# Optimization experiments

Measured on AMD Instinct MI355X. Metric: run time of the kernel, lower is better.

The kernel has to match this reference:

```python
import jax, jax.numpy as jnp
import numpy as np

HEADS = 4
DIM_HEAD = 32


def setup_inputs() -> dict:
    key = jax.random.key(0)
    k1, k2, k3, k4 = jax.random.split(key, 4)
    dim = 64
    hidden = HEADS * DIM_HEAD  # 128
    x = jax.random.normal(k1, (1, dim, 16, 16, 16), jnp.float32)
    # Conv3d 1x1 kernels collapse to [out_ch, in_ch] matrices
    w_qkv = jax.random.normal(k2, (hidden * 3, dim), jnp.float32) * 0.05
    w_out = jax.random.normal(k3, (dim, hidden), jnp.float32) * 0.05
    b_out = jax.random.normal(k4, (dim,), jnp.float32) * 0.05
    return {"x": x, "w_qkv": w_qkv, "w_out": w_out, "b_out": b_out}


def reference(x, w_qkv, w_out, b_out):
    scale = DIM_HEAD ** -0.5
    b, c, dz, dy, dx = x.shape
    n = dz * dy * dx
    xf = x.reshape(b, c, n)  # flatten spatial dims
    # 1x1 Conv3d (no bias) == channel matmul: [b, 3*hidden, n]
    qkv = jnp.einsum('oc,bcn->bon', w_qkv, xf)
    q, k, v = jnp.split(qkv, 3, axis=1)  # each [b, hidden, n]
    def split_heads(t):
        return t.reshape(b, HEADS, DIM_HEAD, n)  # [b, h, d, n]
    q, k, v = split_heads(q), split_heads(k), split_heads(v)
    q = q * scale
    # sim[b,h,i,j] = sum_d q[b,h,d,i] k[b,h,d,j]
    sim = jnp.einsum('bhdi,bhdj->bhij', q, k)
    sim = sim - jax.lax.stop_gradient(jnp.max(sim, axis=-1, keepdims=True))
    attn = jax.nn.softmax(sim, axis=-1)
    # out[b,h,i,d] = sum_j attn[b,h,i,j] v[b,h,d,j]
    out = jnp.einsum('bhij,bhdj->bhid', attn, v)
    # 'b h (z y x) d -> b (h d) z y x'
    out = out.transpose(0, 1, 3, 2).reshape(b, HEADS * DIM_HEAD, n)
    # final 1x1 Conv3d with bias
    y = jnp.einsum('oc,bcn->bon', w_out, out) + b_out[None, :, None]
    return y.reshape(b, -1, dz, dy, dx)
```

## Files before the change

### kernel.cpp

```cpp
#include <hip/hip_runtime.h>


typedef _Float16 f16x8 __attribute__((ext_vector_type(8)));
typedef _Float16 f16x4 __attribute__((ext_vector_type(4)));
typedef _Float16 f16x2v __attribute__((ext_vector_type(2)));
typedef float f32x4 __attribute__((ext_vector_type(4)));

static __device__ inline f16x4 pack4(float a, float b, float c, float d) {
  f16x4 r;
  r.x = (_Float16)a; r.y = (_Float16)b; r.z = (_Float16)c; r.w = (_Float16)d;
  return r;
}
static __device__ inline f16x2v pack2(float a, float b) {
  f16x2v r;
  r.x = (_Float16)a; r.y = (_Float16)b;
  return r;
}

__global__ __launch_bounds__(256) void qkv_kernel(
    const float* __restrict__ x, const float* __restrict__ w,
    _Float16* __restrict__ qo, _Float16* __restrict__ ko, _Float16* __restrict__ vo)
{
  __shared__ __align__(16) float xs[64 * 68];
  __shared__ __align__(16) float wsb[32 * 68];
  const int t = threadIdx.x;
  const int n0 = blockIdx.x * 64;
  const int o0 = blockIdx.y * 32;
  #pragma unroll
  for (int i = 0; i < 4; ++i) {
    int ch = t + i * 256;
    int c = ch >> 4, p = ch & 15;
    *reinterpret_cast<float4*>(&xs[c * 68 + p * 4]) =
        *reinterpret_cast<const float4*>(&x[c * 4096 + n0 + p * 4]);
  }
  #pragma unroll
  for (int i = 0; i < 2; ++i) {
    int ch = t + i * 256;
    int o = ch >> 4, p = ch & 15;
    *reinterpret_cast<float4*>(&wsb[o * 68 + p * 4]) =
        *reinterpret_cast<const float4*>(&w[(o0 + o) * 64 + p * 4]);
  }
  __syncthreads();
  const int oL = (t >> 5) * 4;
  const int nL = (t & 31) * 2;
  float acc[4][2] = {};
  for (int c4 = 0; c4 < 64; c4 += 4) {
    float2 xa[4];
    #pragma unroll
    for (int k = 0; k < 4; ++k)
      xa[k] = *reinterpret_cast<const float2*>(&xs[(c4 + k) * 68 + nL]);
    #pragma unroll
    for (int i = 0; i < 4; ++i) {
      float4 wv = *reinterpret_cast<const float4*>(&wsb[(oL + i) * 68 + c4]);
      acc[i][0] += wv.x * xa[0].x + wv.y * xa[1].x + wv.z * xa[2].x + wv.w * xa[3].x;
      acc[i][1] += wv.x * xa[0].y + wv.y * xa[1].y + wv.z * xa[2].y + wv.w * xa[3].y;
    }
  }
  const float qs = 0.17677669529663689f * 1.4426950408889634f;
  if (o0 < 128) {
    int ho = o0 >> 5;
    #pragma unroll
    for (int j = 0; j < 2; ++j) {
      int n = n0 + nL + j;
      *reinterpret_cast<f16x4*>(&qo[(ho * 4096 + n) * 32 + oL]) =
          pack4(acc[0][j] * qs, acc[1][j] * qs, acc[2][j] * qs, acc[3][j] * qs);
    }
  } else if (o0 < 256) {
    int ho = (o0 - 128) >> 5;
    #pragma unroll
    for (int j = 0; j < 2; ++j) {
      int n = n0 + nL + j;
      *reinterpret_cast<f16x4*>(&ko[(ho * 4096 + n) * 32 + oL]) =
          pack4(acc[0][j], acc[1][j], acc[2][j], acc[3][j]);
    }
  } else {
    #pragma unroll
    for (int i = 0; i < 4; ++i) {
      *reinterpret_cast<f16x2v*>(&vo[(size_t)(o0 - 256 + oL + i) * 4096 + n0 + nL]) =
          pack2(acc[i][0], acc[i][1]);
    }
  }
}

__global__ __launch_bounds__(512, 4) void attn_kernel(
    const _Float16* __restrict__ qg, const _Float16* __restrict__ kg,
    const _Float16* __restrict__ vg, float* __restrict__ Opart,
    float* __restrict__ lpart, int jlen)
{
  __shared__ __align__(16) _Float16 Ks[2][64 * 40];
  __shared__ __align__(16) _Float16 Vs[2][32 * 72];
  const int t = threadIdx.x;
  const int ck = blockIdx.x;
  const int qt = blockIdx.y;
  const int h  = blockIdx.z;
  const int w = t >> 6;
  const int lane = t & 63;
  const int m = lane & 15;
  const int quad = lane >> 4;
  const int qw = qt * 256 + w * 32;

  f16x8 aq[2];
  #pragma unroll
  for (int g = 0; g < 2; ++g)
    aq[g] = *reinterpret_cast<const f16x8*>(
        &qg[(h * 4096 + qw + g * 16 + m) * 32 + quad * 8]);

  f32x4 acc[2][2];
  #pragma unroll
  for (int g = 0; g < 2; ++g) {
    acc[g][0] = f32x4{0.f, 0.f, 0.f, 0.f};
    acc[g][1] = f32x4{0.f, 0.f, 0.f, 0.f};
  }
  float ls[2] = {0.f, 0.f};

  const int jbeg = ck * jlen;
  const bool isK = (t < 256);
  const _Float16* gp;
  int ldsoff;
  if (isK) {
    int kr = t >> 2, ksg = t & 3;
    gp = kg + (size_t)(h * 4096 + jbeg + kr) * 32 + ksg * 8;
    ldsoff = kr * 40 + ksg * 8;
  } else {
    int c = t - 256, vr = c >> 3, vsg = c & 7;
    gp = vg + (size_t)(h * 32 + vr) * 4096 + jbeg + vsg * 8;
    ldsoff = vr * 72 + vsg * 8;
  }

  if (isK)
    *reinterpret_cast<uint4*>(&Ks[0][ldsoff]) = *reinterpret_cast<const uint4*>(gp);
  else
    *reinterpret_cast<uint4*>(&Vs[0][ldsoff]) = *reinterpret_cast<const uint4*>(gp);
  __syncthreads();

  for (int it = 0; it < jlen; it += 64) {
    const int buf = (it >> 6) & 1;
    if (it + 64 < jlen) {
      if (isK)
        *reinterpret_cast<uint4*>(&Ks[buf ^ 1][ldsoff]) =
            *reinterpret_cast<const uint4*>(gp + (size_t)(it + 64) * 32);
      else
        *reinterpret_cast<uint4*>(&Vs[buf ^ 1][ldsoff]) =
            *reinterpret_cast<const uint4*>(gp + (it + 64));
    }
    #pragma unroll
    for (int jt = 0; jt < 4; ++jt) {
      f16x8 kf = *reinterpret_cast<const f16x8*>(&Ks[buf][(jt * 16 + m) * 40 + quad * 8]);
      f16x4 vf0 = *reinterpret_cast<const f16x4*>(&Vs[buf][m * 72 + jt * 16 + quad * 4]);
      f16x4 vf1 = *reinterpret_cast<const f16x4*>(&Vs[buf][(16 + m) * 72 + jt * 16 + quad * 4]);
      f32x4 z = {0.f, 0.f, 0.f, 0.f};
      f32x4 sT[2];
      #pragma unroll
      for (int g = 0; g < 2; ++g)
        sT[g] = __builtin_amdgcn_mfma_f32_16x16x32_f16(kf, aq[g], z, 0, 0, 0);
      #pragma unroll
      for (int g = 0; g < 2; ++g) {
        float p0 = exp2f(sT[g][0]), p1 = exp2f(sT[g][1]);
        float p2 = exp2f(sT[g][2]), p3 = exp2f(sT[g][3]);
        ls[g] += (p0 + p1) + (p2 + p3);
        f16x4 p = pack4(p0, p1, p2, p3);
        acc[g][0] = __builtin_amdgcn_mfma_f32_16x16x16f16(p, vf0, acc[g][0], 0, 0, 0);
        acc[g][1] = __builtin_amdgcn_mfma_f32_16x16x16f16(p, vf1, acc[g][1], 0, 0, 0);
      }
    }
    __syncthreads();
  }

  #pragma unroll
  for (int g = 0; g < 2; ++g) {
    ls[g] += __shfl_xor(ls[g], 16);
    ls[g] += __shfl_xor(ls[g], 32);
  }
  const size_t cb = (size_t)(ck * 4 + h) * 4096;
  #pragma unroll
  for (int g = 0; g < 2; ++g) {
    #pragma unroll
    for (int dt = 0; dt < 2; ++dt) {
      #pragma unroll
      for (int r = 0; r < 4; ++r) {
        int q = qw + g * 16 + quad * 4 + r;
        Opart[(cb + q) * 32 + dt * 16 + m] = acc[g][dt][r];
      }
    }
  }
  if (quad == 0) {
    #pragma unroll
    for (int g = 0; g < 2; ++g)
      lpart[cb + qw + g * 16 + m] = ls[g];
  }
}

__global__ __launch_bounds__(512) void out_kernel(
    const float* __restrict__ Opart, const float* __restrict__ lpart,
    const float* __restrict__ wo, const float* __restrict__ bo,
    float* __restrict__ y)
{
  __shared__ __align__(16) float as[16 * 132];
  __shared__ __align__(16) float wsh[64 * 132];
  __shared__ float linv[64];
  const int t = threadIdx.x;
  const int nb = blockIdx.x * 16;
  if (t < 64) {
    int h = t >> 4, r = t & 15;
    float s = 0.f;
    #pragma unroll
    for (int ck = 0; ck < 8; ++ck)
      s += lpart[(size_t)(ck * 4 + h) * 4096 + nb + r];
    linv[t] = 1.f / s;
  }
  {
    int ch = t;
    #pragma unroll
    for (int i = 0; i < 4; ++i, ch += 512) {
      int r = ch >> 5, p = ch & 31;
      *reinterpret_cast<float4*>(&wsh[r * 132 + p * 4]) =
          *reinterpret_cast<const float4*>(&wo[r * 128 + p * 4]);
    }
  }
  __syncthreads();
  {
    int r = t >> 5, p = t & 31;
    int h = p >> 3, d4 = (p & 7) * 4;
    float4 s = {0.f, 0.f, 0.f, 0.f};
    #pragma unroll
    for (int ck = 0; ck < 8; ++ck) {
      float4 o4 = *reinterpret_cast<const float4*>(
          &Opart[((size_t)(ck * 4 + h) * 4096 + nb + r) * 32 + d4]);
      s.x += o4.x; s.y += o4.y; s.z += o4.z; s.w += o4.w;
    }
    float inv = linv[h * 16 + r];
    s.x *= inv; s.y *= inv; s.z *= inv; s.w *= inv;
    *reinterpret_cast<float4*>(&as[r * 132 + p * 4]) = s;
  }
  __syncthreads();
  const int oL = (t >> 4) * 2;
  const int n = t & 15;
  float acc[2] = {0.f, 0.f};
  for (int c = 0; c < 128; c += 4) {
    float4 a = *reinterpret_cast<const float4*>(&as[n * 132 + c]);
    #pragma unroll
    for (int i = 0; i < 2; ++i) {
      float4 wv = *reinterpret_cast<const float4*>(&wsh[(oL + i) * 132 + c]);
      acc[i] += wv.x * a.x + wv.y * a.y + wv.z * a.z + wv.w * a.w;
    }
  }
  #pragma unroll
  for (int i = 0; i < 2; ++i) {
    y[(size_t)(oL + i) * 4096 + nb + n] = acc[i] + bo[oL + i];
  }
}

extern "C" void kernel_launch(void* const* d_in, const int* in_sizes, int n_in,
                              void* d_out, int out_size, void* d_ws, size_t ws_size,
                              hipStream_t stream) {
  (void)in_sizes; (void)n_in; (void)out_size; (void)ws_size;
  const float* x     = (const float*)d_in[0];
  const float* w_qkv = (const float*)d_in[1];
  const float* w_out = (const float*)d_in[2];
  const float* b_out = (const float*)d_in[3];
  float* y = (float*)d_out;
  _Float16* qb = (_Float16*)d_ws;
  _Float16* kb = qb + 524288;
  _Float16* vb = kb + 524288;
  float* Opart = (float*)(vb + 524288);
  float* lpart = Opart + 4194304;

  qkv_kernel<<<dim3(64, 12), 256, 0, stream>>>(x, w_qkv, qb, kb, vb);
  attn_kernel<<<dim3(8, 16, 4), 512, 0, stream>>>(qb, kb, vb, Opart, lpart, 4096 / 8);
  out_kernel<<<256, 512, 0, stream>>>(Opart, lpart, w_out, b_out, y);
}
```

Baseline: 103.0 us.

## Fuse QKV, attention and output stages into one cooperative persistent kernel

Replaces the three separate launches with one cooperative kernel of 512 blocks that runs the QKV projection, split-K attention and output projection in turn, separated by grid-wide syncs. The aim is to remove launch gaps and per-kernel ramp-up at this small problem size. In exchange, attention now runs with 256-thread blocks handling two work units each instead of the original 512-thread grid, and every grid sync adds cost. If the cooperative launch fails, the code falls back to the three-kernel path.

```diff
diff --git a/kernel.cpp b/kernel.cpp
--- a/kernel.cpp
+++ b/kernel.cpp
@@ -1,4 +1,7 @@
 #include <hip/hip_runtime.h>
+#include <hip/hip_cooperative_groups.h>
+
+namespace cg = cooperative_groups;
 
 
 typedef _Float16 f16x8 __attribute__((ext_vector_type(8)));
@@ -15,6 +18,234 @@
   f16x2v r;
   r.x = (_Float16)a; r.y = (_Float16)b;
   return r;
+}
+
+__global__ __launch_bounds__(256, 4) void fused_kernel(
+    const float* __restrict__ x, const float* __restrict__ wq,
+    const float* __restrict__ wo, const float* __restrict__ bo,
+    float* __restrict__ y,
+    _Float16* __restrict__ qb, _Float16* __restrict__ kb,
+    _Float16* __restrict__ vb,
+    float* __restrict__ Opart, float* __restrict__ lpart)
+{
+  __shared__ __align__(16) char smem[26112];
+  const int t = threadIdx.x;
+  const int bid = blockIdx.x;
+  cg::grid_group grid = cg::this_grid();
+
+  for (int s = 0; s < 2; ++s) {
+    const int unit = bid + s * 512;
+    if (unit >= 768) break;
+    if (s) __syncthreads();
+    float* xs  = (float*)smem;
+    float* wsb = (float*)(smem + 17408);
+    const int n0 = (unit & 63) * 64;
+    const int o0 = (unit >> 6) * 32;
+    #pragma unroll
+    for (int i = 0; i < 4; ++i) {
+      int ch = t + i * 256;
+      int c = ch >> 4, p = ch & 15;
+      *reinterpret_cast<float4*>(&xs[c * 68 + p * 4]) =
+          *reinterpret_cast<const float4*>(&x[c * 4096 + n0 + p * 4]);
+    }
+    #pragma unroll
+    for (int i = 0; i < 2; ++i) {
+      int ch = t + i * 256;
+      int o = ch >> 4, p = ch & 15;
+      *reinterpret_cast<float4*>(&wsb[o * 68 + p * 4]) =
+          *reinterpret_cast<const float4*>(&wq[(o0 + o) * 64 + p * 4]);
+    }
+    __syncthreads();
+    const int oL = (t >> 5) * 4;
+    const int nL = (t & 31) * 2;
+    float acc[4][2] = {};
+    for (int c4 = 0; c4 < 64; c4 += 4) {
+      float2 xa[4];
+      #pragma unroll
+      for (int k = 0; k < 4; ++k)
+        xa[k] = *reinterpret_cast<const float2*>(&xs[(c4 + k) * 68 + nL]);
+      #pragma unroll
+      for (int i = 0; i < 4; ++i) {
+        float4 wv = *reinterpret_cast<const float4*>(&wsb[(oL + i) * 68 + c4]);
+        acc[i][0] += wv.x * xa[0].x + wv.y * xa[1].x + wv.z * xa[2].x + wv.w * xa[3].x;
+        acc[i][1] += wv.x * xa[0].y + wv.y * xa[1].y + wv.z * xa[2].y + wv.w * xa[3].y;
+      }
+    }
+    const float qs = 0.17677669529663689f * 1.4426950408889634f;
+    if (o0 < 128) {
+      int ho = o0 >> 5;
+      #pragma unroll
+      for (int j = 0; j < 2; ++j) {
+        int n = n0 + nL + j;
+        *reinterpret_cast<f16x4*>(&qb[(ho * 4096 + n) * 32 + oL]) =
+            pack4(acc[0][j] * qs, acc[1][j] * qs, acc[2][j] * qs, acc[3][j] * qs);
+      }
+    } else if (o0 < 256) {
+      int ho = (o0 - 128) >> 5;
+      #pragma unroll
+      for (int j = 0; j < 2; ++j) {
+        int n = n0 + nL + j;
+        *reinterpret_cast<f16x4*>(&kb[(ho * 4096 + n) * 32 + oL]) =
+            pack4(acc[0][j], acc[1][j], acc[2][j], acc[3][j]);
+      }
+    } else {
+      #pragma unroll
+      for (int i = 0; i < 4; ++i) {
+        *reinterpret_cast<f16x2v*>(&vb[(size_t)(o0 - 256 + oL + i) * 4096 + n0 + nL]) =
+            pack2(acc[i][0], acc[i][1]);
+      }
+    }
+  }
+
+  __threadfence();
+  grid.sync();
+
+  {
+    _Float16* Ks = (_Float16*)smem;
+    _Float16* Vs = (_Float16*)(smem + 10240);
+    const int wid = t >> 6;
+    const int lane = t & 63;
+    const int m = lane & 15;
+    const int quad = lane >> 4;
+    const int kr = t >> 2, ksg = t & 3;
+    const int vr = t >> 3, vsg = t & 7;
+
+    for (int s = 0; s < 2; ++s) {
+      const int unit = bid + 512 * s;
+      const int ck = unit & 7;
+      const int qt = (unit >> 3) & 31;
+      const int h  = unit >> 8;
+      const int qw = qt * 128 + wid * 32;
+      if (s) __syncthreads();
+
+      f16x8 aq[2];
+      #pragma unroll
+      for (int g = 0; g < 2; ++g)
+        aq[g] = *reinterpret_cast<const f16x8*>(
+            &qb[(h * 4096 + qw + g * 16 + m) * 32 + quad * 8]);
+
+      f32x4 acc[2][2];
+      #pragma unroll
+      for (int g = 0; g < 2; ++g) {
+        acc[g][0] = f32x4{0.f, 0.f, 0.f, 0.f};
+        acc[g][1] = f32x4{0.f, 0.f, 0.f, 0.f};
+      }
+      float ls[2] = {0.f, 0.f};
+
+      const int jbeg = ck * 512;
+      const _Float16* kgp = kb + (size_t)(h * 4096 + jbeg + kr) * 32 + ksg * 8;
+      const _Float16* vgp = vb + (size_t)(h * 32 + vr) * 4096 + jbeg + vsg * 8;
+
+      *reinterpret_cast<uint4*>(&Ks[kr * 40 + ksg * 8]) =
+          *reinterpret_cast<const uint4*>(kgp);
+      *reinterpret_cast<uint4*>(&Vs[vr * 72 + vsg * 8]) =
+          *reinterpret_cast<const uint4*>(vgp);
+      __syncthreads();
+
+      for (int it = 0; it < 512; it += 64) {
+        const int buf = (it >> 6) & 1;
+        if (it + 64 < 512) {
+          *reinterpret_cast<uint4*>(&Ks[(buf ^ 1) * 2560 + kr * 40 + ksg * 8]) =
+              *reinterpret_cast<const uint4*>(kgp + (size_t)(it + 64) * 32);
+          *reinterpret_cast<uint4*>(&Vs[(buf ^ 1) * 2304 + vr * 72 + vsg * 8]) =
+              *reinterpret_cast<const uint4*>(vgp + it + 64);
+        }
+        #pragma unroll
+        for (int jt = 0; jt < 4; ++jt) {
+          f16x8 kf = *reinterpret_cast<const f16x8*>(
+              &Ks[buf * 2560 + (jt * 16 + m) * 40 + quad * 8]);
+          f16x4 vf0 = *reinterpret_cast<const f16x4*>(
+              &Vs[buf * 2304 + m * 72 + jt * 16 + quad * 4]);
+          f16x4 vf1 = *reinterpret_cast<const f16x4*>(
+              &Vs[buf * 2304 + (16 + m) * 72 + jt * 16 + quad * 4]);
+          f32x4 z = {0.f, 0.f, 0.f, 0.f};
+          f32x4 sT[2];
+          #pragma unroll
+          for (int g = 0; g < 2; ++g)
+            sT[g] = __builtin_amdgcn_mfma_f32_16x16x32_f16(kf, aq[g], z, 0, 0, 0);
+          #pragma unroll
+          for (int g = 0; g < 2; ++g) {
+            float p0 = exp2f(sT[g][0]), p1 = exp2f(sT[g][1]);
+            float p2 = exp2f(sT[g][2]), p3 = exp2f(sT[g][3]);
+            ls[g] += (p0 + p1) + (p2 + p3);
+            f16x4 p = pack4(p0, p1, p2, p3);
+            acc[g][0] = __builtin_amdgcn_mfma_f32_16x16x16f16(p, vf0, acc[g][0], 0, 0, 0);
+            acc[g][1] = __builtin_amdgcn_mfma_f32_16x16x16f16(p, vf1, acc[g][1], 0, 0, 0);
+          }
+        }
+        __syncthreads();
+      }
+
+      #pragma unroll
+      for (int g = 0; g < 2; ++g) {
+        ls[g] += __shfl_xor(ls[g], 16);
+        ls[g] += __shfl_xor(ls[g], 32);
+      }
+      const size_t cb = (size_t)(ck * 4 + h) * 4096;
+      #pragma unroll
+      for (int g = 0; g < 2; ++g) {
+        #pragma unroll
+        for (int dt = 0; dt < 2; ++dt) {
+          #pragma unroll
+          for (int r = 0; r < 4; ++r) {
+            int q = qw + g * 16 + quad * 4 + r;
+            Opart[(cb + q) * 32 + dt * 16 + m] = acc[g][dt][r];
+          }
+        }
+      }
+      if (quad == 0) {
+        #pragma unroll
+        for (int g = 0; g < 2; ++g)
+          lpart[cb + qw + g * 16 + m] = ls[g];
+      }
+    }
+  }
+
+  __threadfence();
+  grid.sync();
+
+  {
+    float* as   = (float*)smem;
+    float* linv = (float*)(smem + 4224);
+    const int nb = bid * 8;
+    if (t < 32) {
+      int h2 = t >> 3, r = t & 7;
+      float ssum = 0.f;
+      #pragma unroll
+      for (int ck2 = 0; ck2 < 8; ++ck2)
+        ssum += lpart[(size_t)(ck2 * 4 + h2) * 4096 + nb + r];
+      linv[t] = 1.f / ssum;
+    }
+    __syncthreads();
+    {
+      int r = t >> 5, p = t & 31;
+      int h2 = p >> 3, d4 = (p & 7) * 4;
+      float4 ssum = {0.f, 0.f, 0.f, 0.f};
+      #pragma unroll
+      for (int ck2 = 0; ck2 < 8; ++ck2) {
+        float4 o4 = *reinterpret_cast<const float4*>(
+            &Opart[((size_t)(ck2 * 4 + h2) * 4096 + nb + r) * 32 + d4]);
+        ssum.x += o4.x; ssum.y += o4.y; ssum.z += o4.z; ssum.w += o4.w;
+      }
+      float inv = linv[h2 * 8 + r];
+      ssum.x *= inv; ssum.y *= inv; ssum.z *= inv; ssum.w *= inv;
+      *reinterpret_cast<float4*>(&as[r * 132 + p * 4]) = ssum;
+    }
+    __syncthreads();
+    const int o = t >> 2;
+    const int nn = t & 3;
+    float a0 = 0.f, a1 = 0.f;
+    for (int c = 0; c < 128; c += 4) {
+      float4 wv = *reinterpret_cast<const float4*>(&wo[o * 128 + c]);
+      float4 u0 = *reinterpret_cast<const float4*>(&as[nn * 132 + c]);
+      float4 u1 = *reinterpret_cast<const float4*>(&as[(nn + 4) * 132 + c]);
+      a0 += wv.x * u0.x + wv.y * u0.y + wv.z * u0.z + wv.w * u0.w;
+      a1 += wv.x * u1.x + wv.y * u1.y + wv.z * u1.z + wv.w * u1.w;
+    }
+    const float bias = bo[o];
+    y[(size_t)o * 4096 + nb + nn] = a0 + bias;
+    y[(size_t)o * 4096 + nb + nn + 4] = a1 + bias;
+  }
 }
 
 __global__ __launch_bounds__(256) void qkv_kernel(
@@ -265,7 +496,14 @@
   float* Opart = (float*)(vb + 524288);
   float* lpart = Opart + 4194304;
 
-  qkv_kernel<<<dim3(64, 12), 256, 0, stream>>>(x, w_qkv, qb, kb, vb);
-  attn_kernel<<<dim3(8, 16, 4), 512, 0, stream>>>(qb, kb, vb, Opart, lpart, 4096 / 8);
-  out_kernel<<<256, 512, 0, stream>>>(Opart, lpart, w_out, b_out, y);
-}
+  void* args[] = {(void*)&x, (void*)&w_qkv, (void*)&w_out, (void*)&b_out,
+                  (void*)&y, (void*)&qb, (void*)&kb, (void*)&vb,
+                  (void*)&Opart, (void*)&lpart};
+  hipError_t err = hipLaunchCooperativeKernel((const void*)fused_kernel,
+                                              dim3(512), dim3(256), args, 0, stream);
+  if (err != hipSuccess) {
+    qkv_kernel<<<dim3(64, 12), 256, 0, stream>>>(x, w_qkv, qb, kb, vb);
+    attn_kernel<<<dim3(8, 16, 4), 512, 0, stream>>>(qb, kb, vb, Opart, lpart, 4096 / 8);
+    out_kernel<<<256, 512, 0, stream>>>(Opart, lpart, w_out, b_out, y);
+  }
+}
```

After: 372.4 us. 3.61x slower.
